# Kernel tuning notes

Hardware: AMD Instinct MI355X
Metric: run time of the kernel (lower is better)

Reference implementation:

```python
import jax, jax.numpy as jnp
import numpy as np

WS = 7          # window_size[0]
UP = 2          # hardcoded upscale
WS2 = WS * UP   # 14
NUM_HEADS = 6
DIM = 192
HEAD_DIM = DIM // NUM_HEADS
SCALE = HEAD_DIM ** -0.5
TABLE_SIZE = (WS + WS2 - 1) ** 2  # 400


def _relative_position_index():
    # Mirrors the torch __init__ index construction (meshgrid 'ij').
    ch = np.arange(WS)
    cw = np.arange(WS2)
    r1, c1 = np.meshgrid(ch, ch, indexing='ij')   # (7,7)
    r2, c2 = np.meshgrid(cw, cw, indexing='ij')   # (14,14)
    r1, c1 = r1.reshape(-1), c1.reshape(-1)       # (49,)
    r2, c2 = r2.reshape(-1), c2.reshape(-1)       # (196,)
    rel_row = r1[:, None] - r2[None, :] + (WS2 - 1)          # (49,196) in [0,19]
    rel_col = c1[:, None] - c2[None, :] + (WS2 - 1)
    idx = rel_row * (WS + WS2 - 1) + rel_col                 # (49,196) in [0,399]
    return jnp.asarray(idx, dtype=jnp.int32)

REL_INDEX = _relative_position_index()


def setup_inputs() -> dict:
    key = jax.random.key(0)
    ks = jax.random.split(key, 9)
    B, N, N2, C = 1024, WS * WS, WS2 * WS2, DIM
    std = 0.02
    return {
        'x1': jax.random.normal(ks[0], (B, N, C), jnp.float32),
        'x2': jax.random.normal(ks[1], (B, N2, C), jnp.float32),
        # Linear weights stored as (in, out) so y = x @ W + b
        'qkv_w': jax.random.normal(ks[2], (C, C), jnp.float32) * std,
        'qkv_b': jnp.zeros((C,), jnp.float32),
        'qkv2_w': jax.random.normal(ks[3], (C, 2 * C), jnp.float32) * std,
        'qkv2_b': jnp.zeros((2 * C,), jnp.float32),
        'proj_w': jax.random.normal(ks[4], (C, C), jnp.float32) * std,
        'proj_b': jnp.zeros((C,), jnp.float32),
        'bias_table': jax.random.normal(ks[5], (TABLE_SIZE, NUM_HEADS), jnp.float32) * std,
    }


def reference(x1, x2, qkv_w, qkv_b, qkv2_w, qkv2_b, proj_w, proj_b, bias_table):
    B, N, C = x1.shape
    _, N2, _ = x2.shape
    H, D = NUM_HEADS, HEAD_DIM

    q = (x1 @ qkv_w + qkv_b).reshape(B, N, H, D).transpose(0, 2, 1, 3)        # [B,H,N,D]
    kv = (x2 @ qkv2_w + qkv2_b).reshape(B, N2, 2, H, D).transpose(2, 0, 3, 1, 4)
    k, v = kv[0], kv[1]                                                        # [B,H,N2,D]

    attn = jnp.einsum('bhnd,bhmd->bhnm', q * SCALE, k)                         # [B,H,N,N2]
    bias = bias_table[REL_INDEX].transpose(2, 0, 1)                            # [H,N,N2]
    attn = jax.nn.softmax(attn + bias[None], axis=-1)

    out = jnp.einsum('bhnm,bhmd->bhnd', attn, v).transpose(0, 2, 1, 3).reshape(B, N, C)
    return out @ proj_w + proj_b
```

## Files before the change

kernel.cpp:

```cpp
#include <hip/hip_runtime.h>


typedef __attribute__((ext_vector_type(8))) short bf16x8;
typedef __attribute__((ext_vector_type(4))) float f32x4;

#define MFMA16(a, b, c) __builtin_amdgcn_mfma_f32_16x16x32_bf16((a), (b), (c), 0, 0, 0)

#define WS_QKVT  0
#define WS_QKV2T 36864
#define WS_PROJH 110592
#define WS_PROJL 147456

#define SCALE_Q 0.17677669529663687f

__device__ __forceinline__ unsigned short f2bf(float f) {
  unsigned int u = __float_as_uint(f);
  u += 0x7fffu + ((u >> 16) & 1u);
  return (unsigned short)(u >> 16);
}
__device__ __forceinline__ float bf2f(unsigned short s) {
  return __uint_as_float(((unsigned int)s) << 16);
}
__device__ __forceinline__ bf16x8 cvt8(const float* __restrict__ p) {
  union { bf16x8 v; unsigned short s[8]; } U;
  float4 v0 = *(const float4*)p;
  float4 v1 = *(const float4*)(p + 4);
  U.s[0] = f2bf(v0.x); U.s[1] = f2bf(v0.y); U.s[2] = f2bf(v0.z); U.s[3] = f2bf(v0.w);
  U.s[4] = f2bf(v1.x); U.s[5] = f2bf(v1.y); U.s[6] = f2bf(v1.z); U.s[7] = f2bf(v1.w);
  return U.v;
}

__global__ void prep_kernel(const float* __restrict__ qkv_w,
                            const float* __restrict__ qkv2_w,
                            const float* __restrict__ proj_w,
                            unsigned short* __restrict__ ws) {
  int t = blockIdx.x * 256 + threadIdx.x;
  if (t < 36864) {
    int k = t / 192, n = t % 192;
    ws[WS_QKVT + n * 192 + k] = f2bf(qkv_w[t]);
  } else if (t < 110592) {
    int u = t - 36864;
    int k = u / 384, n = u % 384;
    ws[WS_QKV2T + n * 192 + k] = f2bf(qkv2_w[u]);
  } else if (t < 147456) {
    int u = t - 110592;
    int k = u / 192, n = u % 192;
    float p = proj_w[u];
    unsigned short hi = f2bf(p);
    ws[WS_PROJH + n * 192 + k] = hi;
    ws[WS_PROJL + n * 192 + k] = f2bf(p - bf2f(hi));
  }
}

__launch_bounds__(256, 2)
__global__ void attn_kernel(const float* __restrict__ x1,
                            const float* __restrict__ x2,
                            const float* __restrict__ qkv_b,
                            const float* __restrict__ qkv2_b,
                            const float* __restrict__ btab,
                            const unsigned short* __restrict__ ws,
                            float* __restrict__ out) {
  extern __shared__ char smem[];
  unsigned short* ksm = (unsigned short*)(smem);
  unsigned short* vtm = (unsigned short*)(smem + 15680);
  unsigned short* atm = (unsigned short*)(smem + 30528);
  unsigned short* qhm = (unsigned short*)(smem + 60224);

  const int tid  = threadIdx.x;
  const int wave = tid >> 6;
  const int lane = tid & 63;
  const int l16  = lane & 15;
  const int quad = lane >> 4;
  const int b    = blockIdx.x;

  const float* x1b = x1 + (size_t)b * (49 * 192);
  const float* x2b = x2 + (size_t)b * (196 * 192);

  {
    int* z = (int*)(smem + 30528);
    for (int i = tid; i < 29696 / 4; i += 256) z[i] = 0;
    int* z2 = (int*)(smem + 15680);
    for (int i = tid; i < 14848 / 4; i += 256) z2[i] = 0;
  }

  int Pr[4];
#pragma unroll
  for (int r = 0; r < 4; ++r) {
    int i = wave * 16 + quad * 4 + r;
    if (i > 48) i = 48;
    int ih = i / 7, iw = i - 7 * ih;
    Pr[r] = ih * 20 + iw + 273;
  }

  __syncthreads();

  for (int h = 0; h < 6; ++h) {
    {
      f32x4 acc0{0.f, 0.f, 0.f, 0.f}, acc1{0.f, 0.f, 0.f, 0.f};
      const int m = wave * 16 + l16;
      const bool mv = (m < 49);
#pragma unroll
      for (int kk = 0; kk < 6; ++kk) {
        const int k0 = kk * 32 + quad * 8;
        bf16x8 a;
        if (mv) a = cvt8(x1b + m * 192 + k0);
        else    a = bf16x8{0, 0, 0, 0, 0, 0, 0, 0};
        const unsigned short* wq = ws + WS_QKVT + (h * 32 + l16) * 192 + k0;
        acc0 = MFMA16(a, *(const bf16x8*)(wq), acc0);
        acc1 = MFMA16(a, *(const bf16x8*)(wq + 16 * 192), acc1);
      }
      const float bia0 = qkv_b[h * 32 + l16];
      const float bia1 = qkv_b[h * 32 + 16 + l16];
#pragma unroll
      for (int r = 0; r < 4; ++r) {
        const int row = wave * 16 + quad * 4 + r;
        qhm[row * 40 + l16]      = f2bf((acc0[r] + bia0) * SCALE_Q);
        qhm[row * 40 + 16 + l16] = f2bf((acc1[r] + bia1) * SCALE_Q);
      }
    }
    for (int mt = wave; mt < 13; mt += 4) {
      f32x4 acc0{0.f, 0.f, 0.f, 0.f}, acc1{0.f, 0.f, 0.f, 0.f};
      f32x4 acc2{0.f, 0.f, 0.f, 0.f}, acc3{0.f, 0.f, 0.f, 0.f};
      const int m = mt * 16 + l16;
      const bool mv = (m < 196);
#pragma unroll
      for (int kk = 0; kk < 6; ++kk) {
        const int k0 = kk * 32 + quad * 8;
        bf16x8 a;
        if (mv) a = cvt8(x2b + m * 192 + k0);
        else    a = bf16x8{0, 0, 0, 0, 0, 0, 0, 0};
        const unsigned short* wk = ws + WS_QKV2T + (h * 32 + l16) * 192 + k0;
        acc0 = MFMA16(a, *(const bf16x8*)(wk), acc0);
        acc1 = MFMA16(a, *(const bf16x8*)(wk + 16 * 192), acc1);
        acc2 = MFMA16(a, *(const bf16x8*)(wk + 192 * 192), acc2);
        acc3 = MFMA16(a, *(const bf16x8*)(wk + 208 * 192), acc3);
      }
      const float bk0 = qkv2_b[h * 32 + l16];
      const float bk1 = qkv2_b[h * 32 + 16 + l16];
      const float bv0 = qkv2_b[192 + h * 32 + l16];
      const float bv1 = qkv2_b[192 + h * 32 + 16 + l16];
#pragma unroll
      for (int r = 0; r < 4; ++r) {
        const int row = mt * 16 + quad * 4 + r;
        if (row < 196) {
          ksm[row * 40 + l16]      = f2bf(acc0[r] + bk0);
          ksm[row * 40 + 16 + l16] = f2bf(acc1[r] + bk1);
        }
        vtm[l16 * 232 + row]        = f2bf(acc2[r] + bv0);
        vtm[(16 + l16) * 232 + row] = f2bf(acc3[r] + bv1);
      }
    }
    __syncthreads();

    f32x4 lg[13];
    {
      const int m = wave * 16 + l16;
      bf16x8 a = *(const bf16x8*)(qhm + m * 40 + quad * 8);
#pragma unroll
      for (int nt = 0; nt < 13; ++nt) {
        bf16x8 bb = *(const bf16x8*)(ksm + (nt * 16 + l16) * 40 + quad * 8);
        lg[nt] = MFMA16(a, bb, (f32x4{0.f, 0.f, 0.f, 0.f}));
      }
#pragma unroll
      for (int nt = 0; nt < 13; ++nt) {
        const int jc = nt * 16 + l16;
        if (jc < 196) {
          const int jh = jc / 14, jw = jc - 14 * jh;
          const int qj = jh * 20 + jw;
#pragma unroll
          for (int r = 0; r < 4; ++r) lg[nt][r] += btab[(Pr[r] - qj) * 6 + h];
        } else {
#pragma unroll
          for (int r = 0; r < 4; ++r) lg[nt][r] = -1e30f;
        }
      }
#pragma unroll
      for (int r = 0; r < 4; ++r) {
        float mx = lg[0][r];
#pragma unroll
        for (int nt = 1; nt < 13; ++nt) mx = fmaxf(mx, lg[nt][r]);
        mx = fmaxf(mx, __shfl_xor(mx, 1));
        mx = fmaxf(mx, __shfl_xor(mx, 2));
        mx = fmaxf(mx, __shfl_xor(mx, 4));
        mx = fmaxf(mx, __shfl_xor(mx, 8));
        float s = 0.f;
#pragma unroll
        for (int nt = 0; nt < 13; ++nt) {
          float p = __expf(lg[nt][r] - mx);
          lg[nt][r] = p;
          s += p;
        }
        s += __shfl_xor(s, 1);
        s += __shfl_xor(s, 2);
        s += __shfl_xor(s, 4);
        s += __shfl_xor(s, 8);
        const float inv = 1.f / s;
        const int row = wave * 16 + quad * 4 + r;
        if (row < 49) {
#pragma unroll
          for (int nt = 0; nt < 13; ++nt)
            atm[row * 232 + nt * 16 + l16] = f2bf(lg[nt][r] * inv);
        }
      }
    }
    {
      f32x4 o0{0.f, 0.f, 0.f, 0.f}, o1{0.f, 0.f, 0.f, 0.f};
      const int m = wave * 16 + l16;
#pragma unroll
      for (int kk = 0; kk < 7; ++kk) {
        const int k0 = kk * 32 + quad * 8;
        bf16x8 a  = *(const bf16x8*)(atm + m * 232 + k0);
        bf16x8 b0 = *(const bf16x8*)(vtm + l16 * 232 + k0);
        bf16x8 b1 = *(const bf16x8*)(vtm + (16 + l16) * 232 + k0);
        o0 = MFMA16(a, b0, o0);
        o1 = MFMA16(a, b1, o1);
      }
#pragma unroll
      for (int r = 0; r < 4; ++r) {
        const int row = wave * 16 + quad * 4 + r;
        if (row < 49) {
          float* op = out + (size_t)b * 9408 + row * 192 + h * 32;
          op[l16]      = o0[r];
          op[16 + l16] = o1[r];
        }
      }
    }
    __syncthreads();
  }
}

__launch_bounds__(256, 2)
__global__ void proj_kernel(const float* __restrict__ proj_b,
                            const unsigned short* __restrict__ ws,
                            float* __restrict__ out) {
  extern __shared__ char smem[];
  float* aout = (float*)smem;
  const int tid  = threadIdx.x;
  const int wave = tid >> 6;
  const int lane = tid & 63;
  const int l16  = lane & 15;
  const int quad = lane >> 4;
  const size_t base = (size_t)blockIdx.x * 64 * 192;

  for (int i = tid; i < 64 * 192 / 4; i += 256) {
    int row = i / 48, col = (i - row * 48) * 4;
    float4 v = *(const float4*)(out + base + row * 192 + col);
    *(float4*)(aout + row * 204 + col) = v;
  }
  __syncthreads();

  f32x4 pacc[12];
#pragma unroll
  for (int nt = 0; nt < 12; ++nt) pacc[nt] = f32x4{0.f, 0.f, 0.f, 0.f};

  const int m = wave * 16 + l16;
#pragma unroll
  for (int kk = 0; kk < 6; ++kk) {
    const int k0 = kk * 32 + quad * 8;
    const float* ap = aout + m * 204 + k0;
    float4 v0 = *(const float4*)ap;
    float4 v1 = *(const float4*)(ap + 4);
    float f[8] = {v0.x, v0.y, v0.z, v0.w, v1.x, v1.y, v1.z, v1.w};
    union { bf16x8 v; unsigned short s[8]; } H, L;
#pragma unroll
    for (int j = 0; j < 8; ++j) {
      H.s[j] = f2bf(f[j]);
      L.s[j] = f2bf(f[j] - bf2f(H.s[j]));
    }
#pragma unroll
    for (int nt = 0; nt < 12; ++nt) {
      const unsigned short* bph = ws + WS_PROJH + (nt * 16 + l16) * 192 + k0;
      const unsigned short* bpl = ws + WS_PROJL + (nt * 16 + l16) * 192 + k0;
      bf16x8 bh = *(const bf16x8*)bph;
      bf16x8 bl = *(const bf16x8*)bpl;
      pacc[nt] = MFMA16(H.v, bh, pacc[nt]);
      pacc[nt] = MFMA16(H.v, bl, pacc[nt]);
      pacc[nt] = MFMA16(L.v, bh, pacc[nt]);
    }
  }
#pragma unroll
  for (int nt = 0; nt < 12; ++nt) {
    const float pb = proj_b[nt * 16 + l16];
#pragma unroll
    for (int r = 0; r < 4; ++r) {
      const int row = wave * 16 + quad * 4 + r;
      out[base + row * 192 + nt * 16 + l16] = pacc[nt][r] + pb;
    }
  }
}

extern "C" void kernel_launch(void* const* d_in, const int* in_sizes, int n_in,
                              void* d_out, int out_size, void* d_ws, size_t ws_size,
                              hipStream_t stream) {
  const float* x1     = (const float*)d_in[0];
  const float* x2     = (const float*)d_in[1];
  const float* qkv_w  = (const float*)d_in[2];
  const float* qkv_b  = (const float*)d_in[3];
  const float* qkv2_w = (const float*)d_in[4];
  const float* qkv2_b = (const float*)d_in[5];
  const float* proj_w = (const float*)d_in[6];
  const float* proj_b = (const float*)d_in[7];
  const float* btab   = (const float*)d_in[8];
  unsigned short* ws  = (unsigned short*)d_ws;
  float* out          = (float*)d_out;
  (void)in_sizes; (void)n_in; (void)out_size; (void)ws_size;

  prep_kernel<<<dim3(576), dim3(256), 0, stream>>>(qkv_w, qkv2_w, proj_w, ws);
  attn_kernel<<<dim3(1024), dim3(256), 65344, stream>>>(x1, x2, qkv_b, qkv2_b,
                                                        btab, ws, out);
  proj_kernel<<<dim3(784), dim3(256), 52224, stream>>>(proj_b, ws, out);
}
```

Measured before the change: 668.9 us.

## Fuse output projection into attention kernel and use 512-thread blocks

Merges the projection GEMM into the attention kernel, so per-head outputs stay in registers and shared memory and are never written to and reread from global memory. Blocks grow to 8 waves: x2 rows are converted to bf16 once into registers and reused across all heads, and the softmax is split across two waves per row tile, combining max and sum through shared memory. This removes one kernel launch and a full global round trip of the intermediate, and stops the per-head reconversion of x2. In exchange it adds extra barriers per head and much higher register pressure from the cached x2 fragments and six output accumulators, which may limit occupancy under the 512-thread launch bound.

```diff
diff --git a/kernel.cpp b/kernel.cpp
--- a/kernel.cpp
+++ b/kernel.cpp
@@ -52,12 +52,76 @@
   }
 }
 
-__launch_bounds__(256, 2)
+__device__ __forceinline__ void kv_tile(const bf16x8* fr, int t, int h,
+                                        const unsigned short* __restrict__ ws,
+                                        const float* __restrict__ qkv2_b,
+                                        unsigned short* ksm, unsigned short* vtm,
+                                        int l16, int quad) {
+  f32x4 a0{0.f,0.f,0.f,0.f}, a1{0.f,0.f,0.f,0.f};
+  f32x4 a2{0.f,0.f,0.f,0.f}, a3{0.f,0.f,0.f,0.f};
+  const unsigned short* wb = ws + WS_QKV2T + (h * 32 + l16) * 192;
+#pragma unroll
+  for (int kk = 0; kk < 6; ++kk) {
+    const int k0 = kk * 32 + quad * 8;
+    bf16x8 b0 = *(const bf16x8*)(wb + k0);
+    bf16x8 b1 = *(const bf16x8*)(wb + 16 * 192 + k0);
+    bf16x8 b2 = *(const bf16x8*)(wb + 192 * 192 + k0);
+    bf16x8 b3 = *(const bf16x8*)(wb + 208 * 192 + k0);
+    a0 = MFMA16(fr[kk], b0, a0);
+    a1 = MFMA16(fr[kk], b1, a1);
+    a2 = MFMA16(fr[kk], b2, a2);
+    a3 = MFMA16(fr[kk], b3, a3);
+  }
+  const float bk0 = qkv2_b[h * 32 + l16];
+  const float bk1 = qkv2_b[h * 32 + 16 + l16];
+  const float bv0 = qkv2_b[192 + h * 32 + l16];
+  const float bv1 = qkv2_b[192 + h * 32 + 16 + l16];
+#pragma unroll
+  for (int r = 0; r < 4; ++r) {
+    const int row = t * 16 + quad * 4 + r;
+    if (row < 196) {
+      ksm[row * 40 + l16]      = f2bf(a0[r] + bk0);
+      ksm[row * 40 + 16 + l16] = f2bf(a1[r] + bk1);
+    }
+    vtm[l16 * 232 + row]        = f2bf(a2[r] + bv0);
+    vtm[(16 + l16) * 232 + row] = f2bf(a3[r] + bv1);
+  }
+}
+
+__device__ __forceinline__ void q_tile(int qt, int h,
+                                       const float* __restrict__ x1b,
+                                       const unsigned short* __restrict__ ws,
+                                       const float* __restrict__ qkv_b,
+                                       unsigned short* qhm, int l16, int quad) {
+  const bf16x8 ZV = {0,0,0,0,0,0,0,0};
+  f32x4 a0{0.f,0.f,0.f,0.f}, a1{0.f,0.f,0.f,0.f};
+  const int m = qt * 16 + l16;
+  const bool mv = (m < 49);
+  const unsigned short* wq = ws + WS_QKVT + (h * 32 + l16) * 192;
+#pragma unroll
+  for (int kk = 0; kk < 6; ++kk) {
+    const int k0 = kk * 32 + quad * 8;
+    bf16x8 a = mv ? cvt8(x1b + m * 192 + k0) : ZV;
+    a0 = MFMA16(a, *(const bf16x8*)(wq + k0), a0);
+    a1 = MFMA16(a, *(const bf16x8*)(wq + 16 * 192 + k0), a1);
+  }
+  const float b0 = qkv_b[h * 32 + l16];
+  const float b1 = qkv_b[h * 32 + 16 + l16];
+#pragma unroll
+  for (int r = 0; r < 4; ++r) {
+    const int row = qt * 16 + quad * 4 + r;
+    qhm[row * 40 + l16]      = f2bf((a0[r] + b0) * SCALE_Q);
+    qhm[row * 40 + 16 + l16] = f2bf((a1[r] + b1) * SCALE_Q);
+  }
+}
+
+__launch_bounds__(512, 4)
 __global__ void attn_kernel(const float* __restrict__ x1,
                             const float* __restrict__ x2,
                             const float* __restrict__ qkv_b,
                             const float* __restrict__ qkv2_b,
                             const float* __restrict__ btab,
+                            const float* __restrict__ proj_b,
                             const unsigned short* __restrict__ ws,
                             float* __restrict__ out) {
   extern __shared__ char smem[];
@@ -65,6 +129,8 @@
   unsigned short* vtm = (unsigned short*)(smem + 15680);
   unsigned short* atm = (unsigned short*)(smem + 30528);
   unsigned short* qhm = (unsigned short*)(smem + 60224);
+  unsigned short* oh  = (unsigned short*)(smem);
+  unsigned short* ol  = (unsigned short*)(smem + 25600);
 
   const int tid  = threadIdx.x;
   const int wave = tid >> 6;
@@ -73,218 +139,201 @@
   const int quad = lane >> 4;
   const int b    = blockIdx.x;
 
-  const float* x1b = x1 + (size_t)b * (49 * 192);
-  const float* x2b = x2 + (size_t)b * (196 * 192);
+  const float* x1b = x1 + (size_t)b * 9408;
+  const float* x2b = x2 + (size_t)b * 37632;
+
+  const bf16x8 ZV = {0,0,0,0,0,0,0,0};
+  bf16x8 xf[12];
+  const int t0 = wave;
+  const int t1 = (wave < 4) ? wave + 8 : ((wave == 4) ? 12 : -1);
+  {
+    const int m0 = t0 * 16 + l16;
+#pragma unroll
+    for (int kk = 0; kk < 6; ++kk)
+      xf[kk] = (m0 < 196) ? cvt8(x2b + m0 * 192 + kk * 32 + quad * 8) : ZV;
+    if (t1 >= 0) {
+      const int m1 = t1 * 16 + l16;
+#pragma unroll
+      for (int kk = 0; kk < 6; ++kk)
+        xf[6 + kk] = (m1 < 196) ? cvt8(x2b + m1 * 192 + kk * 32 + quad * 8) : ZV;
+    } else {
+#pragma unroll
+      for (int kk = 0; kk < 6; ++kk) xf[6 + kk] = ZV;
+    }
+  }
 
   {
     int* z = (int*)(smem + 30528);
-    for (int i = tid; i < 29696 / 4; i += 256) z[i] = 0;
+    for (int i = tid; i < 29696 / 4; i += 512) z[i] = 0;
     int* z2 = (int*)(smem + 15680);
-    for (int i = tid; i < 14848 / 4; i += 256) z2[i] = 0;
-  }
-
+    for (int i = tid; i < 14848 / 4; i += 512) z2[i] = 0;
+  }
+
+  const int mt2 = (wave >= 4) ? wave - 4 : wave;
+  const int ntb = (wave >= 4) ? 0 : 7;
+  const int g   = (wave >= 4) ? 0 : 1;
   int Pr[4];
 #pragma unroll
   for (int r = 0; r < 4; ++r) {
-    int i = wave * 16 + quad * 4 + r;
+    int i = mt2 * 16 + quad * 4 + r;
     if (i > 48) i = 48;
     int ih = i / 7, iw = i - 7 * ih;
     Pr[r] = ih * 20 + iw + 273;
   }
+  int Qj[7];  bool Jv[7];
+#pragma unroll
+  for (int j = 0; j < 7; ++j) {
+    const int nt = ntb + j;
+    const int jc = nt * 16 + l16;
+    Jv[j] = (nt <= 12) && (jc < 196);
+    const int jcc = (jc < 196) ? jc : 195;
+    const int jh = jcc / 14, jw = jcc - 14 * jh;
+    Qj[j] = jh * 20 + jw;
+  }
 
   __syncthreads();
 
+  f32x4 o[6];
+
+#pragma unroll
   for (int h = 0; h < 6; ++h) {
+    kv_tile(xf, t0, h, ws, qkv2_b, ksm, vtm, l16, quad);
+    if (t1 >= 0) kv_tile(xf + 6, t1, h, ws, qkv2_b, ksm, vtm, l16, quad);
+    if (wave == 5) q_tile(0, h, x1b, ws, qkv_b, qhm, l16, quad);
+    if (wave == 6) q_tile(1, h, x1b, ws, qkv_b, qhm, l16, quad);
+    if (wave == 7) { q_tile(2, h, x1b, ws, qkv_b, qhm, l16, quad);
+                     q_tile(3, h, x1b, ws, qkv_b, qhm, l16, quad); }
+    __syncthreads();
+
+    f32x4 lg[7];
     {
-      f32x4 acc0{0.f, 0.f, 0.f, 0.f}, acc1{0.f, 0.f, 0.f, 0.f};
-      const int m = wave * 16 + l16;
-      const bool mv = (m < 49);
-#pragma unroll
-      for (int kk = 0; kk < 6; ++kk) {
-        const int k0 = kk * 32 + quad * 8;
-        bf16x8 a;
-        if (mv) a = cvt8(x1b + m * 192 + k0);
-        else    a = bf16x8{0, 0, 0, 0, 0, 0, 0, 0};
-        const unsigned short* wq = ws + WS_QKVT + (h * 32 + l16) * 192 + k0;
-        acc0 = MFMA16(a, *(const bf16x8*)(wq), acc0);
-        acc1 = MFMA16(a, *(const bf16x8*)(wq + 16 * 192), acc1);
-      }
-      const float bia0 = qkv_b[h * 32 + l16];
-      const float bia1 = qkv_b[h * 32 + 16 + l16];
-#pragma unroll
-      for (int r = 0; r < 4; ++r) {
-        const int row = wave * 16 + quad * 4 + r;
-        qhm[row * 40 + l16]      = f2bf((acc0[r] + bia0) * SCALE_Q);
-        qhm[row * 40 + 16 + l16] = f2bf((acc1[r] + bia1) * SCALE_Q);
-      }
-    }
-    for (int mt = wave; mt < 13; mt += 4) {
-      f32x4 acc0{0.f, 0.f, 0.f, 0.f}, acc1{0.f, 0.f, 0.f, 0.f};
-      f32x4 acc2{0.f, 0.f, 0.f, 0.f}, acc3{0.f, 0.f, 0.f, 0.f};
-      const int m = mt * 16 + l16;
-      const bool mv = (m < 196);
-#pragma unroll
-      for (int kk = 0; kk < 6; ++kk) {
-        const int k0 = kk * 32 + quad * 8;
-        bf16x8 a;
-        if (mv) a = cvt8(x2b + m * 192 + k0);
-        else    a = bf16x8{0, 0, 0, 0, 0, 0, 0, 0};
-        const unsigned short* wk = ws + WS_QKV2T + (h * 32 + l16) * 192 + k0;
-        acc0 = MFMA16(a, *(const bf16x8*)(wk), acc0);
-        acc1 = MFMA16(a, *(const bf16x8*)(wk + 16 * 192), acc1);
-        acc2 = MFMA16(a, *(const bf16x8*)(wk + 192 * 192), acc2);
-        acc3 = MFMA16(a, *(const bf16x8*)(wk + 208 * 192), acc3);
-      }
-      const float bk0 = qkv2_b[h * 32 + l16];
-      const float bk1 = qkv2_b[h * 32 + 16 + l16];
-      const float bv0 = qkv2_b[192 + h * 32 + l16];
-      const float bv1 = qkv2_b[192 + h * 32 + 16 + l16];
-#pragma unroll
-      for (int r = 0; r < 4; ++r) {
-        const int row = mt * 16 + quad * 4 + r;
-        if (row < 196) {
-          ksm[row * 40 + l16]      = f2bf(acc0[r] + bk0);
-          ksm[row * 40 + 16 + l16] = f2bf(acc1[r] + bk1);
-        }
-        vtm[l16 * 232 + row]        = f2bf(acc2[r] + bv0);
-        vtm[(16 + l16) * 232 + row] = f2bf(acc3[r] + bv1);
-      }
-    }
-    __syncthreads();
-
-    f32x4 lg[13];
-    {
-      const int m = wave * 16 + l16;
-      bf16x8 a = *(const bf16x8*)(qhm + m * 40 + quad * 8);
-#pragma unroll
-      for (int nt = 0; nt < 13; ++nt) {
-        bf16x8 bb = *(const bf16x8*)(ksm + (nt * 16 + l16) * 40 + quad * 8);
-        lg[nt] = MFMA16(a, bb, (f32x4{0.f, 0.f, 0.f, 0.f}));
-      }
-#pragma unroll
-      for (int nt = 0; nt < 13; ++nt) {
-        const int jc = nt * 16 + l16;
-        if (jc < 196) {
-          const int jh = jc / 14, jw = jc - 14 * jh;
-          const int qj = jh * 20 + jw;
-#pragma unroll
-          for (int r = 0; r < 4; ++r) lg[nt][r] += btab[(Pr[r] - qj) * 6 + h];
+      bf16x8 aq = *(const bf16x8*)(qhm + (mt2 * 16 + l16) * 40 + quad * 8);
+#pragma unroll
+      for (int j = 0; j < 7; ++j) {
+        const int nt = ntb + j;
+        if (nt <= 12) {
+          bf16x8 bb = *(const bf16x8*)(ksm + (nt * 16 + l16) * 40 + quad * 8);
+          lg[j] = MFMA16(aq, bb, (f32x4{0.f, 0.f, 0.f, 0.f}));
+          if (Jv[j]) {
+#pragma unroll
+            for (int r = 0; r < 4; ++r) lg[j][r] += btab[(Pr[r] - Qj[j]) * 6 + h];
+          } else {
+#pragma unroll
+            for (int r = 0; r < 4; ++r) lg[j][r] = -1e30f;
+          }
         } else {
 #pragma unroll
-          for (int r = 0; r < 4; ++r) lg[nt][r] = -1e30f;
+          for (int r = 0; r < 4; ++r) lg[j][r] = -1e30f;
         }
       }
 #pragma unroll
       for (int r = 0; r < 4; ++r) {
         float mx = lg[0][r];
 #pragma unroll
-        for (int nt = 1; nt < 13; ++nt) mx = fmaxf(mx, lg[nt][r]);
+        for (int j = 1; j < 7; ++j) mx = fmaxf(mx, lg[j][r]);
         mx = fmaxf(mx, __shfl_xor(mx, 1));
         mx = fmaxf(mx, __shfl_xor(mx, 2));
         mx = fmaxf(mx, __shfl_xor(mx, 4));
         mx = fmaxf(mx, __shfl_xor(mx, 8));
-        float s = 0.f;
-#pragma unroll
-        for (int nt = 0; nt < 13; ++nt) {
-          float p = __expf(lg[nt][r] - mx);
-          lg[nt][r] = p;
-          s += p;
+        if (l16 == 0) {
+          const int row = mt2 * 16 + quad * 4 + r;
+          *(float*)(qhm + row * 40 + 32 + 2 * g) = mx;
         }
-        s += __shfl_xor(s, 1);
-        s += __shfl_xor(s, 2);
-        s += __shfl_xor(s, 4);
-        s += __shfl_xor(s, 8);
-        const float inv = 1.f / s;
-        const int row = wave * 16 + quad * 4 + r;
-        if (row < 49) {
-#pragma unroll
-          for (int nt = 0; nt < 13; ++nt)
-            atm[row * 232 + nt * 16 + l16] = f2bf(lg[nt][r] * inv);
+      }
+    }
+    __syncthreads();
+
+#pragma unroll
+    for (int r = 0; r < 4; ++r) {
+      const int row = mt2 * 16 + quad * 4 + r;
+      const float* sc = (const float*)(qhm + row * 40 + 32);
+      const float gm = fmaxf(sc[0], sc[1]);
+      float s = 0.f;
+#pragma unroll
+      for (int j = 0; j < 7; ++j) {
+        float p = __expf(lg[j][r] - gm);
+        lg[j][r] = p;
+        s += p;
+      }
+      s += __shfl_xor(s, 1);
+      s += __shfl_xor(s, 2);
+      s += __shfl_xor(s, 4);
+      s += __shfl_xor(s, 8);
+      if (l16 == 0) *(float*)(qhm + row * 40 + 36 + 2 * g) = s;
+      if (row < 49) {
+#pragma unroll
+        for (int j = 0; j < 7; ++j) {
+          const int jc = (ntb + j) * 16 + l16;
+          atm[row * 232 + jc] = f2bf(lg[j][r]);
         }
       }
     }
+    __syncthreads();
+
     {
-      f32x4 o0{0.f, 0.f, 0.f, 0.f}, o1{0.f, 0.f, 0.f, 0.f};
-      const int m = wave * 16 + l16;
+      const int mt3 = wave >> 1, half = wave & 1;
+      f32x4 t{0.f, 0.f, 0.f, 0.f};
 #pragma unroll
       for (int kk = 0; kk < 7; ++kk) {
         const int k0 = kk * 32 + quad * 8;
-        bf16x8 a  = *(const bf16x8*)(atm + m * 232 + k0);
-        bf16x8 b0 = *(const bf16x8*)(vtm + l16 * 232 + k0);
-        bf16x8 b1 = *(const bf16x8*)(vtm + (16 + l16) * 232 + k0);
-        o0 = MFMA16(a, b0, o0);
-        o1 = MFMA16(a, b1, o1);
+        bf16x8 a = *(const bf16x8*)(atm + (mt3 * 16 + l16) * 232 + k0);
+        bf16x8 v = *(const bf16x8*)(vtm + (half * 16 + l16) * 232 + k0);
+        t = MFMA16(a, v, t);
       }
 #pragma unroll
       for (int r = 0; r < 4; ++r) {
-        const int row = wave * 16 + quad * 4 + r;
-        if (row < 49) {
-          float* op = out + (size_t)b * 9408 + row * 192 + h * 32;
-          op[l16]      = o0[r];
-          op[16 + l16] = o1[r];
-        }
+        const int row = mt3 * 16 + quad * 4 + r;
+        const float* sc = (const float*)(qhm + row * 40 + 32);
+        o[h][r] = t[r] * __frcp_rn(sc[2] + sc[3]);
       }
     }
     __syncthreads();
   }
-}
-
-__launch_bounds__(256, 2)
-__global__ void proj_kernel(const float* __restrict__ proj_b,
-                            const unsigned short* __restrict__ ws,
-                            float* __restrict__ out) {
-  extern __shared__ char smem[];
-  float* aout = (float*)smem;
-  const int tid  = threadIdx.x;
-  const int wave = tid >> 6;
-  const int lane = tid & 63;
-  const int l16  = lane & 15;
-  const int quad = lane >> 4;
-  const size_t base = (size_t)blockIdx.x * 64 * 192;
-
-  for (int i = tid; i < 64 * 192 / 4; i += 256) {
-    int row = i / 48, col = (i - row * 48) * 4;
-    float4 v = *(const float4*)(out + base + row * 192 + col);
-    *(float4*)(aout + row * 204 + col) = v;
+
+  {
+    const int mt3 = wave >> 1, half = wave & 1;
+#pragma unroll
+    for (int h2 = 0; h2 < 6; ++h2)
+#pragma unroll
+      for (int r = 0; r < 4; ++r) {
+        const int row = mt3 * 16 + quad * 4 + r;
+        const int col = h2 * 32 + half * 16 + l16;
+        const float v = o[h2][r];
+        const unsigned short hi = f2bf(v);
+        oh[row * 200 + col] = hi;
+        ol[row * 200 + col] = f2bf(v - bf2f(hi));
+      }
   }
   __syncthreads();
-
-  f32x4 pacc[12];
-#pragma unroll
-  for (int nt = 0; nt < 12; ++nt) pacc[nt] = f32x4{0.f, 0.f, 0.f, 0.f};
-
-  const int m = wave * 16 + l16;
-#pragma unroll
-  for (int kk = 0; kk < 6; ++kk) {
-    const int k0 = kk * 32 + quad * 8;
-    const float* ap = aout + m * 204 + k0;
-    float4 v0 = *(const float4*)ap;
-    float4 v1 = *(const float4*)(ap + 4);
-    float f[8] = {v0.x, v0.y, v0.z, v0.w, v1.x, v1.y, v1.z, v1.w};
-    union { bf16x8 v; unsigned short s[8]; } H, L;
-#pragma unroll
-    for (int j = 0; j < 8; ++j) {
-      H.s[j] = f2bf(f[j]);
-      L.s[j] = f2bf(f[j] - bf2f(H.s[j]));
-    }
-#pragma unroll
-    for (int nt = 0; nt < 12; ++nt) {
-      const unsigned short* bph = ws + WS_PROJH + (nt * 16 + l16) * 192 + k0;
-      const unsigned short* bpl = ws + WS_PROJL + (nt * 16 + l16) * 192 + k0;
-      bf16x8 bh = *(const bf16x8*)bph;
-      bf16x8 bl = *(const bf16x8*)bpl;
-      pacc[nt] = MFMA16(H.v, bh, pacc[nt]);
-      pacc[nt] = MFMA16(H.v, bl, pacc[nt]);
-      pacc[nt] = MFMA16(L.v, bh, pacc[nt]);
-    }
-  }
-#pragma unroll
-  for (int nt = 0; nt < 12; ++nt) {
-    const float pb = proj_b[nt * 16 + l16];
-#pragma unroll
-    for (int r = 0; r < 4; ++r) {
-      const int row = wave * 16 + quad * 4 + r;
-      out[base + row * 192 + nt * 16 + l16] = pacc[nt][r] + pb;
+  {
+    const int mtp = wave & 3;
+    const int nb  = (wave < 4) ? 0 : 6;
+    f32x4 pacc[6];
+#pragma unroll
+    for (int j = 0; j < 6; ++j) pacc[j] = f32x4{0.f, 0.f, 0.f, 0.f};
+#pragma unroll
+    for (int kk = 0; kk < 6; ++kk) {
+      const int k0 = kk * 32 + quad * 8;
+      bf16x8 ah = *(const bf16x8*)(oh + (mtp * 16 + l16) * 200 + k0);
+      bf16x8 al = *(const bf16x8*)(ol + (mtp * 16 + l16) * 200 + k0);
+#pragma unroll
+      for (int j = 0; j < 6; ++j) {
+        const unsigned short* bh = ws + WS_PROJH + ((nb + j) * 16 + l16) * 192 + k0;
+        const unsigned short* bl = ws + WS_PROJL + ((nb + j) * 16 + l16) * 192 + k0;
+        pacc[j] = MFMA16(ah, *(const bf16x8*)bh, pacc[j]);
+        pacc[j] = MFMA16(ah, *(const bf16x8*)bl, pacc[j]);
+        pacc[j] = MFMA16(al, *(const bf16x8*)bh, pacc[j]);
+      }
+    }
+#pragma unroll
+    for (int j = 0; j < 6; ++j) {
+      const float pb = proj_b[(nb + j) * 16 + l16];
+#pragma unroll
+      for (int r = 0; r < 4; ++r) {
+        const int row = mtp * 16 + quad * 4 + r;
+        if (row < 49)
+          out[(size_t)b * 9408 + row * 192 + (nb + j) * 16 + l16] = pacc[j][r] + pb;
+      }
     }
   }
 }
@@ -306,7 +355,6 @@
   (void)in_sizes; (void)n_in; (void)out_size; (void)ws_size;
 
   prep_kernel<<<dim3(576), dim3(256), 0, stream>>>(qkv_w, qkv2_w, proj_w, ws);
-  attn_kernel<<<dim3(1024), dim3(256), 65344, stream>>>(x1, x2, qkv_b, qkv2_b,
-                                                        btab, ws, out);
-  proj_kernel<<<dim3(784), dim3(256), 52224, stream>>>(proj_b, ws, out);
-}
+  attn_kernel<<<dim3(1024), dim3(512), 65344, stream>>>(x1, x2, qkv_b, qkv2_b,
+                                                        btab, proj_b, ws, out);
+}
```

Measured after the change: 1.676 ms. 151% more time.
